# Kernel tuning notes

Hardware: AMD Instinct MI355X
Metric: run time of the kernel (lower is better)

## Reference

```python
import jax, jax.numpy as jnp
import numpy as np

B, N, C, H = 8, 1025, 768, 12
HD = C // H  # 64
SCALE = HD ** -0.5


def rotate_half(x):
    x1, x2 = jnp.split(x, 2, axis=-1)
    return jnp.concatenate((-x2, x1), axis=-1)


def apply_rope(x, sin, cos):
    return x * cos + rotate_half(x) * sin


def setup_inputs() -> dict:
    key = jax.random.key(0)
    ks = jax.random.split(key, 7)
    x = jax.random.normal(ks[0], (B, N, C), dtype=jnp.float32)
    sin = jax.random.normal(ks[1], (N - 1, HD), dtype=jnp.float32)
    cos = jax.random.normal(ks[2], (N - 1, HD), dtype=jnp.float32)
    s = 1.0 / np.sqrt(C)
    qkv_w = jax.random.normal(ks[3], (3 * C, C), dtype=jnp.float32) * s
    qkv_b = jnp.zeros((3 * C,), dtype=jnp.float32)
    proj_w = jax.random.normal(ks[4], (C, C), dtype=jnp.float32) * s
    proj_b = jnp.zeros((C,), dtype=jnp.float32)
    return {"x": x, "sin": sin, "cos": cos, "qkv_w": qkv_w, "qkv_b": qkv_b,
            "proj_w": proj_w, "proj_b": proj_b}


def reference(x, sin, cos, qkv_w, qkv_b, proj_w, proj_b):
    b, n, c = x.shape
    qkv = x @ qkv_w.T + qkv_b                      # [B,N,3C]
    qkv = qkv.reshape(b, n, 3, H, HD)
    qkv = jnp.transpose(qkv, (2, 0, 3, 1, 4))      # [3,B,H,N,HD]
    q, k, v = qkv[0], qkv[1], qkv[2]
    # RoPE on patch tokens only (cls token at index 0 excluded)
    q_patch = apply_rope(q[:, :, 1:, :], sin, cos)
    k_patch = apply_rope(k[:, :, 1:, :], sin, cos)
    q = jnp.concatenate((q[:, :, :1, :], q_patch), axis=2)
    k = jnp.concatenate((k[:, :, :1, :], k_patch), axis=2)
    attn = jnp.einsum('bhqd,bhkd->bhqk', q, k) * SCALE
    attn = jax.nn.softmax(attn, axis=-1)
    out = jnp.einsum('bhqk,bhkd->bhqd', attn, v)   # [B,H,N,HD]
    out = jnp.transpose(out, (0, 2, 1, 3)).reshape(b, n, c)
    out = out @ proj_w.T + proj_b
    return out
```

## Files before the change

### kernel.cpp

```cpp
#include <hip/hip_runtime.h>
#include <hip/hip_bf16.h>

constexpr int NTOK   = 1025;
constexpr int M      = 8 * NTOK;
constexpr int MP     = 8320;
constexpr int KDIM   = 768;
constexpr int NQKV   = 2304;
constexpr int NKVPAD = 1088;
constexpr float SCALEL2 = 0.125f * 1.44269504f;

using bf16x8 = __attribute__((ext_vector_type(8))) short;
using f32x4  = __attribute__((ext_vector_type(4))) float;

__device__ __forceinline__ f32x4 mfma_bf16(bf16x8 a, bf16x8 b, f32x4 c) {
  return __builtin_amdgcn_mfma_f32_16x16x32_bf16(a, b, c, 0, 0, 0);
}

__device__ __forceinline__ void gl16(const void* g, void* l) {
  __builtin_amdgcn_global_load_lds(
      (const __attribute__((address_space(1))) void*)g,
      (__attribute__((address_space(3))) void*)l, 16, 0, 0);
}

template <int N> __device__ __forceinline__ void wait_vmcnt() {
  if constexpr (N == 0)
    asm volatile("s_waitcnt vmcnt(0)" ::: "memory");
  else if constexpr (N == 4)
    asm volatile("s_waitcnt vmcnt(4)" ::: "memory");
  else if constexpr (N == 6)
    asm volatile("s_waitcnt vmcnt(6)" ::: "memory");
}

__device__ __forceinline__ float exp2_raw(float x) {
  float r;
  asm("v_exp_f32 %0, %1" : "=v"(r) : "v"(x));
  return r;
}
__device__ __forceinline__ __hip_bfloat16 cvt_bf16_raw(float x) {
  unsigned u;
  asm("v_cvt_pk_bf16_f32 %0, %1, %2" : "=v"(u) : "v"(x), "v"(x));
  union { unsigned short s; __hip_bfloat16 b; } c;
  c.s = (unsigned short)(u & 0xffffu);
  return c.b;
}

constexpr size_t SZ_X     = (size_t)MP * KDIM * 2;
constexpr size_t SZ_WQ    = (size_t)NQKV * KDIM * 2;
constexpr size_t SZ_PW    = (size_t)KDIM * KDIM * 2;
constexpr size_t SZ_QK    = (size_t)96 * NTOK * 64 * 2;
constexpr size_t SZ_VT    = (size_t)96 * 64 * NKVPAD * 2;
constexpr size_t OFF_XHI  = 0;
constexpr size_t OFF_XLO  = OFF_XHI + SZ_X;
constexpr size_t OFF_WQHI = OFF_XLO + SZ_X;
constexpr size_t OFF_PWHI = OFF_WQHI + SZ_WQ;
constexpr size_t OFF_PWLO = OFF_PWHI + SZ_PW;
constexpr size_t OFF_Q    = OFF_PWLO + SZ_PW;
constexpr size_t OFF_K    = OFF_Q + SZ_QK;
constexpr size_t OFF_VT   = OFF_K + SZ_QK;
constexpr size_t OFF_AO   = OFF_VT + SZ_VT;

__global__ void k_split(const float* __restrict__ src, __hip_bfloat16* __restrict__ hi,
                        __hip_bfloat16* __restrict__ lo, int n_src, int n_dst) {
  int i = blockIdx.x * 256 + threadIdx.x;
  if (i >= n_dst) return;
  float v = (i < n_src) ? src[i] : 0.0f;
  __hip_bfloat16 h = __float2bfloat16(v);
  hi[i] = h;
  lo[i] = __float2bfloat16(v - __bfloat162float(h));
}

__global__ void k_tobf16(const float* __restrict__ src, __hip_bfloat16* __restrict__ dst,
                         int n_src, int n_dst) {
  int i = blockIdx.x * 256 + threadIdx.x;
  if (i >= n_dst) return;
  dst[i] = __float2bfloat16((i < n_src) ? src[i] : 0.0f);
}

__global__ void k_zero_vt(__hip_bfloat16* __restrict__ vt) {
  int i = blockIdx.x * 256 + threadIdx.x;
  constexpr int NPADC = NKVPAD - NTOK;
  if (i >= 96 * 64 * NPADC) return;
  int r = i / NPADC;
  int c = NTOK + (i - r * NPADC);
  vt[(size_t)r * NKVPAD + c] = __float2bfloat16(0.0f);
}

template <int EPI, int NT, int NBX>
__global__ __launch_bounds__(256) void k_gemm(
    const __hip_bfloat16* __restrict__ Ahi, const __hip_bfloat16* __restrict__ Asec,
    const __hip_bfloat16* __restrict__ Bhi, const float* __restrict__ bias,
    const float* __restrict__ sinp, const float* __restrict__ cosp,
    __hip_bfloat16* __restrict__ o_q, __hip_bfloat16* __restrict__ o_k,
    __hip_bfloat16* __restrict__ o_vt, float* __restrict__ o_f32) {
  const int tid = threadIdx.x;
  const int w = tid >> 6, lane = tid & 63;
  const int wm = w >> 1, wn = w & 1;
  const int l15 = lane & 15, q4 = lane >> 4;

  const int nwg = gridDim.x;
  const int orig = blockIdx.x;
  const int qc = nwg >> 3, rc = nwg & 7;
  const int xcd = orig & 7, o8 = orig >> 3;
  const int wg =
      (xcd < rc ? xcd * (qc + 1) : rc * (qc + 1) + (xcd - rc) * qc) + o8;
  const int bx = wg % NBX, by = wg / NBX;
  const int mBase = by * 128, nBase = bx * 128;

  __shared__ __hip_bfloat16 sm[3][NT * 4096];
  constexpr int OFFB = (NT - 1) * 8192;

  const char* p0 = (const char*)Ahi + (size_t)mBase * (KDIM * 2);
  const char* p1 = (const char*)Asec + (size_t)nBase * (KDIM * 2);
  const char* p2 = (const char*)Bhi + (size_t)nBase * (KDIM * 2);

  const int slog = ((tid & 3) ^ ((tid >> 3) & 3)) << 4;
  const int ph = ((q4 ^ ((l15 >> 1) & 3)) << 4);

  auto stage = [&](int kt, int buf) {
    const int kofs = kt * 64;
    char* base = (char*)sm[buf];
#pragma unroll
    for (int i = 0; i < 2; ++i) {
      const int c = i * 256 + tid;
      const size_t rb = (size_t)(i * 64 + (tid >> 2)) * (KDIM * 2) + slog + kofs;
      gl16(p0 + rb, base + (size_t)c * 16);
      if (NT == 3) gl16(p1 + rb, base + 8192 + (size_t)c * 16);
      gl16(p2 + rb, base + OFFB + (size_t)c * 16);
    }
  };

  f32x4 acc[4][4] = {};

  stage(0, 0);
  stage(1, 1);

  constexpr int NKT = KDIM / 32;
  for (int kt = 0; kt < NKT; ++kt) {
    if (kt < NKT - 1)
      wait_vmcnt<2 * NT>();
    else
      wait_vmcnt<0>();
    __builtin_amdgcn_s_barrier();
    if (kt + 2 < NKT) stage(kt + 2, (kt + 2) % 3);
    char* s0 = (char*)sm[kt % 3];
    char* s1 = s0 + 8192;
    char* s2 = s0 + OFFB;
    bf16x8 a0[4], b0[4], b1[4];
#pragma unroll
    for (int mt = 0; mt < 4; ++mt) {
      const int r = wm * 64 + mt * 16 + l15;
      a0[mt] = *(const bf16x8*)(s0 + r * 64 + ph);
    }
#pragma unroll
    for (int nt = 0; nt < 4; ++nt) {
      const int r = wn * 64 + nt * 16 + l15;
      b0[nt] = *(const bf16x8*)(s2 + r * 64 + ph);
      if (NT == 3) b1[nt] = *(const bf16x8*)(s1 + r * 64 + ph);
    }
    __builtin_amdgcn_s_setprio(1);
#pragma unroll
    for (int mt = 0; mt < 4; ++mt)
#pragma unroll
      for (int nt = 0; nt < 4; ++nt) {
        acc[mt][nt] = mfma_bf16(a0[mt], b0[nt], acc[mt][nt]);
        if (NT == 3) acc[mt][nt] = mfma_bf16(a0[mt], b1[nt], acc[mt][nt]);
      }
    __builtin_amdgcn_s_setprio(0);
  }

#pragma unroll
  for (int mt = 0; mt < 4; ++mt)
#pragma unroll
    for (int j = 0; j < 4; ++j) {
      const int gm = mBase + wm * 64 + mt * 16 + q4 * 4 + j;
      if (gm >= M) continue;
      if (EPI == 0) {
        const int b = gm / NTOK;
        const int t = gm - b * NTOK;
#pragma unroll
        for (int nt = 0; nt < 4; ++nt) {
          const int gc = nBase + wn * 64 + nt * 16 + l15;
          float v = acc[mt][nt][j] + bias[gc];
          const int three = gc / 768;
          const int hd = gc - three * 768;
          const int h = hd >> 6, d = hd & 63;
          const int bh = b * 12 + h;
          if (three == 2) {
            o_vt[((size_t)bh * 64 + d) * NKVPAD + t] = __float2bfloat16(v);
          } else {
            if (t > 0) {
              const float pv = acc[mt][nt ^ 2][j] + bias[gc ^ 32];
              const int so = (t - 1) * 64 + d;
              v = v * cosp[so] + ((d < 32) ? -pv : pv) * sinp[so];
            }
            if (three == 0)
              o_q[((size_t)bh * NTOK + t) * 64 + d] = __float2bfloat16(v);
            else
              o_k[((size_t)bh * NTOK + t) * 64 + d] = __float2bfloat16(v * SCALEL2);
          }
        }
      } else {
#pragma unroll
        for (int nt = 0; nt < 4; ++nt) {
          const int gc = nBase + wn * 64 + nt * 16 + l15;
          o_f32[(size_t)gm * 768 + gc] = acc[mt][nt][j] + bias[gc];
        }
      }
    }
}

__global__ __launch_bounds__(256) void k_attn(
    const __hip_bfloat16* __restrict__ Q, const __hip_bfloat16* __restrict__ Kk,
    const __hip_bfloat16* __restrict__ VT, __hip_bfloat16* __restrict__ ao) {
  __shared__ __hip_bfloat16 Kt[3][64 * 64];
  __shared__ __hip_bfloat16 Vt[3][64 * 64];
  __shared__ __hip_bfloat16 Pl[4][32][72];
  const int tid = threadIdx.x, w = tid >> 6, lane = tid & 63;
  const int l15 = lane & 15, q4 = lane >> 4;
  const int id = blockIdx.x;
  const int xcd = id & 7, sub = id >> 3;
  const int hh = sub / 9;
  const int bh = xcd * 12 + hh;
  const int qb = (sub - hh * 9) * 128 + w * 32;
  const size_t qbase = (size_t)bh * NTOK * 64;
  const char* Kb = (const char*)(Kk + qbase);
  const char* Vb = (const char*)(VT + (size_t)bh * 64 * NKVPAD);

  int frag_off[2][4];
#pragma unroll
  for (int f = 0; f < 4; ++f) {
    const int row = f * 16 + l15;
#pragma unroll
    for (int ks = 0; ks < 2; ++ks)
      frag_off[ks][f] = row * 128 + (((ks * 4 + q4) ^ (row & 7)) << 4);
  }
  int stRow[2], sch16[2], stK[2], stV[2], ldsOff[2];
#pragma unroll
  for (int i = 0; i < 2; ++i) {
    const int c = i * 256 + tid;
    const int row = c >> 3;
    stRow[i] = row;
    sch16[i] = ((c & 7) ^ (row & 7)) << 4;
    stK[i] = row * 128 + sch16[i];
    stV[i] = row * (NKVPAD * 2) + sch16[i];
    ldsOff[i] = c * 16;
  }
  int pw_off[2][4], pa_off[2][2];
#pragma unroll
  for (int mt = 0; mt < 2; ++mt) {
#pragma unroll
    for (int j = 0; j < 4; ++j)
      pw_off[mt][j] = ((w * 32 + mt * 16 + q4 * 4 + j) * 72 + l15) * 2;
#pragma unroll
    for (int ks = 0; ks < 2; ++ks)
      pa_off[mt][ks] = ((w * 32 + mt * 16 + l15) * 72 + ks * 32 + q4 * 8) * 2;
  }
  char* Plc = (char*)&Pl[0][0][0];

  bf16x8 qa[2][2];
#pragma unroll
  for (int mt = 0; mt < 2; ++mt) {
    int t = qb + mt * 16 + l15;
    if (t > NTOK - 1) t = NTOK - 1;
#pragma unroll
    for (int ks = 0; ks < 2; ++ks)
      qa[mt][ks] = *(const bf16x8*)(Q + qbase + (size_t)t * 64 + ks * 32 + q4 * 8);
  }

  f32x4 accO[2][4] = {};
  float mrun[2][4], lpart[2][4];
#pragma unroll
  for (int mt = 0; mt < 2; ++mt)
#pragma unroll
    for (int j = 0; j < 4; ++j) {
      mrun[mt][j] = -1e30f;
      lpart[mt][j] = 0.0f;
    }

  auto stageKV = [&](int kt, int b) {
    const int kb0 = kt * 64;
#pragma unroll
    for (int i = 0; i < 2; ++i) {
      const char* srcK;
      if (kt == 16) {
        const int srow = min(kb0 + stRow[i], NTOK - 1);
        srcK = Kb + (size_t)srow * 128 + sch16[i];
      } else {
        srcK = Kb + (size_t)kb0 * 128 + stK[i];
      }
      gl16(srcK, (char*)&Kt[b][0] + ldsOff[i]);
      gl16(Vb + (size_t)kb0 * 2 + stV[i], (char*)&Vt[b][0] + ldsOff[i]);
    }
  };

  auto step = [&](int kt, int cur, bool last) {
    f32x4 s[2][4] = {};
    {
      const char* Kc = (const char*)&Kt[cur][0];
      bf16x8 kfr[2][4];
#pragma unroll
      for (int nt = 0; nt < 4; ++nt)
#pragma unroll
        for (int ks = 0; ks < 2; ++ks)
          kfr[ks][nt] = *(const bf16x8*)(Kc + frag_off[ks][nt]);
      __builtin_amdgcn_s_setprio(1);
#pragma unroll
      for (int mt = 0; mt < 2; ++mt)
#pragma unroll
        for (int nt = 0; nt < 4; ++nt)
#pragma unroll
          for (int ks = 0; ks < 2; ++ks)
            s[mt][nt] = mfma_bf16(qa[mt][ks], kfr[ks][nt], s[mt][nt]);
      __builtin_amdgcn_s_setprio(0);
    }
    if (last) {
#pragma unroll
      for (int nt = 0; nt < 4; ++nt)
        if (1024 + nt * 16 + l15 > NTOK - 1) {
#pragma unroll
          for (int mt = 0; mt < 2; ++mt)
#pragma unroll
            for (int j = 0; j < 4; ++j) s[mt][nt][j] = -1e30f;
        }
    }
    float smax[2][4];
    bool okl = true;
#pragma unroll
    for (int mt = 0; mt < 2; ++mt)
#pragma unroll
      for (int j = 0; j < 4; ++j) {
        const float a =
            fmaxf(fmaxf(s[mt][0][j], s[mt][1][j]), fmaxf(s[mt][2][j], s[mt][3][j]));
        smax[mt][j] = a;
        okl = okl && (a <= mrun[mt][j] + 8.0f);
      }
    if (!__all((int)okl)) {
#pragma unroll
      for (int mt = 0; mt < 2; ++mt)
#pragma unroll
        for (int j = 0; j < 4; ++j) {
          float m0 = smax[mt][j];
#pragma unroll
          for (int off = 1; off < 16; off <<= 1) m0 = fmaxf(m0, __shfl_xor(m0, off));
          const float mnew = fmaxf(mrun[mt][j], m0);
          const float fsc = exp2_raw(mrun[mt][j] - mnew);
          lpart[mt][j] *= fsc;
          mrun[mt][j] = mnew;
#pragma unroll
          for (int nd = 0; nd < 4; ++nd) accO[mt][nd][j] *= fsc;
        }
    }
#pragma unroll
    for (int mt = 0; mt < 2; ++mt)
#pragma unroll
      for (int j = 0; j < 4; ++j) {
        float acc = 0.0f;
        char* pw = Plc + pw_off[mt][j];
#pragma unroll
        for (int nt = 0; nt < 4; ++nt) {
          const float p = exp2_raw(s[mt][nt][j] - mrun[mt][j]);
          acc += p;
          *(__hip_bfloat16*)(pw + nt * 32) = cvt_bf16_raw(p);
        }
        lpart[mt][j] += acc;
      }
    bf16x8 pa[2][2], vf[2][4];
#pragma unroll
    for (int mt = 0; mt < 2; ++mt)
#pragma unroll
      for (int ks = 0; ks < 2; ++ks)
        pa[mt][ks] = *(const bf16x8*)(Plc + pa_off[mt][ks]);
    {
      const char* Vc = (const char*)&Vt[cur][0];
#pragma unroll
      for (int nd = 0; nd < 4; ++nd)
#pragma unroll
        for (int ks = 0; ks < 2; ++ks)
          vf[ks][nd] = *(const bf16x8*)(Vc + frag_off[ks][nd]);
    }
    __builtin_amdgcn_s_setprio(1);
#pragma unroll
    for (int mt = 0; mt < 2; ++mt)
#pragma unroll
      for (int nd = 0; nd < 4; ++nd)
#pragma unroll
        for (int ks = 0; ks < 2; ++ks)
          accO[mt][nd] = mfma_bf16(pa[mt][ks], vf[ks][nd], accO[mt][nd]);
    __builtin_amdgcn_s_setprio(0);
  };

  stageKV(0, 0);
  stageKV(1, 1);
  for (int kt = 0; kt < 17; ++kt) {
    if (kt < 16)
      wait_vmcnt<4>();
    else
      wait_vmcnt<0>();
    __builtin_amdgcn_s_barrier();
    if (kt + 2 < 17) stageKV(kt + 2, (kt + 2) % 3);
    step(kt, kt % 3, kt == 16);
  }

  const int b = bh / 12, h = bh - (bh / 12) * 12;
#pragma unroll
  for (int mt = 0; mt < 2; ++mt)
#pragma unroll
    for (int j = 0; j < 4; ++j) {
      float sum = lpart[mt][j];
#pragma unroll
      for (int off2 = 1; off2 < 16; off2 <<= 1) sum += __shfl_xor(sum, off2);
      const int t = qb + mt * 16 + q4 * 4 + j;
      if (t > NTOK - 1) continue;
      const float inv = 1.0f / sum;
      const size_t ro = ((size_t)(b * NTOK + t)) * 768 + h * 64;
#pragma unroll
      for (int nd = 0; nd < 4; ++nd) {
        const int d = nd * 16 + l15;
        ao[ro + d] = __float2bfloat16(accO[mt][nd][j] * inv);
      }
    }
}

extern "C" void kernel_launch(void* const* d_in, const int* in_sizes, int n_in,
                              void* d_out, int out_size, void* d_ws, size_t ws_size,
                              hipStream_t stream) {
  const float* x = (const float*)d_in[0];
  const float* sinp = (const float*)d_in[1];
  const float* cosp = (const float*)d_in[2];
  const float* qkvw = (const float*)d_in[3];
  const float* qkvb = (const float*)d_in[4];
  const float* projw = (const float*)d_in[5];
  const float* projb = (const float*)d_in[6];

  char* ws = (char*)d_ws;
  __hip_bfloat16* xhi = (__hip_bfloat16*)(ws + OFF_XHI);
  __hip_bfloat16* wqhi = (__hip_bfloat16*)(ws + OFF_WQHI);
  __hip_bfloat16* pwhi = (__hip_bfloat16*)(ws + OFF_PWHI);
  __hip_bfloat16* pwlo = (__hip_bfloat16*)(ws + OFF_PWLO);
  __hip_bfloat16* qb = (__hip_bfloat16*)(ws + OFF_Q);
  __hip_bfloat16* kb = (__hip_bfloat16*)(ws + OFF_K);
  __hip_bfloat16* vt = (__hip_bfloat16*)(ws + OFF_VT);
  __hip_bfloat16* ao = (__hip_bfloat16*)(ws + OFF_AO);

  {
    int n_src = M * KDIM, n_dst = MP * KDIM;
    k_tobf16<<<(n_dst + 255) / 256, 256, 0, stream>>>(x, xhi, n_src, n_dst);
    int nw = NQKV * KDIM;
    k_tobf16<<<(nw + 255) / 256, 256, 0, stream>>>(qkvw, wqhi, nw, nw);
    int np = KDIM * KDIM;
    k_split<<<(np + 255) / 256, 256, 0, stream>>>(projw, pwhi, pwlo, np, np);
    int nz = 96 * 64 * (NKVPAD - NTOK);
    k_zero_vt<<<(nz + 255) / 256, 256, 0, stream>>>(vt);
  }
  k_gemm<0, 2, 18><<<dim3(18 * 65), 256, 0, stream>>>(
      xhi, xhi, wqhi, qkvb, sinp, cosp, qb, kb, vt, nullptr);
  k_attn<<<dim3(864), 256, 0, stream>>>(qb, kb, vt, ao);
  k_gemm<1, 3, 6><<<dim3(6 * 65), 256, 0, stream>>>(
      ao, pwlo, pwhi, projb, nullptr, nullptr, nullptr, nullptr, nullptr,
      (float*)d_out);
}
```

Measured before the change: 223.0 us.

## Fuse prep kernels into one vectorized pass and retile QKV GEMM with K=64 stages

```diff
diff --git a/kernel.cpp b/kernel.cpp
--- a/kernel.cpp
+++ b/kernel.cpp
@@ -36,11 +36,14 @@
   asm("v_exp_f32 %0, %1" : "=v"(r) : "v"(x));
   return r;
 }
-__device__ __forceinline__ __hip_bfloat16 cvt_bf16_raw(float x) {
+__device__ __forceinline__ unsigned short cvt_bf16_u16(float x) {
   unsigned u;
   asm("v_cvt_pk_bf16_f32 %0, %1, %2" : "=v"(u) : "v"(x), "v"(x));
+  return (unsigned short)(u & 0xffffu);
+}
+__device__ __forceinline__ __hip_bfloat16 cvt_bf16_raw(float x) {
   union { unsigned short s; __hip_bfloat16 b; } c;
-  c.s = (unsigned short)(u & 0xffffu);
+  c.s = cvt_bf16_u16(x);
   return c.b;
 }
 
@@ -59,39 +62,67 @@
 constexpr size_t OFF_VT   = OFF_K + SZ_QK;
 constexpr size_t OFF_AO   = OFF_VT + SZ_VT;
 
-__global__ void k_split(const float* __restrict__ src, __hip_bfloat16* __restrict__ hi,
-                        __hip_bfloat16* __restrict__ lo, int n_src, int n_dst) {
-  int i = blockIdx.x * 256 + threadIdx.x;
-  if (i >= n_dst) return;
-  float v = (i < n_src) ? src[i] : 0.0f;
-  __hip_bfloat16 h = __float2bfloat16(v);
-  hi[i] = h;
-  lo[i] = __float2bfloat16(v - __bfloat162float(h));
-}
-
-__global__ void k_tobf16(const float* __restrict__ src, __hip_bfloat16* __restrict__ dst,
-                         int n_src, int n_dst) {
-  int i = blockIdx.x * 256 + threadIdx.x;
-  if (i >= n_dst) return;
-  dst[i] = __float2bfloat16((i < n_src) ? src[i] : 0.0f);
-}
-
-__global__ void k_zero_vt(__hip_bfloat16* __restrict__ vt) {
-  int i = blockIdx.x * 256 + threadIdx.x;
-  constexpr int NPADC = NKVPAD - NTOK;
-  if (i >= 96 * 64 * NPADC) return;
-  int r = i / NPADC;
-  int c = NTOK + (i - r * NPADC);
-  vt[(size_t)r * NKVPAD + c] = __float2bfloat16(0.0f);
-}
-
-template <int EPI, int NT, int NBX>
-__global__ __launch_bounds__(256) void k_gemm(
-    const __hip_bfloat16* __restrict__ Ahi, const __hip_bfloat16* __restrict__ Asec,
-    const __hip_bfloat16* __restrict__ Bhi, const float* __restrict__ bias,
-    const float* __restrict__ sinp, const float* __restrict__ cosp,
-    __hip_bfloat16* __restrict__ o_q, __hip_bfloat16* __restrict__ o_k,
-    __hip_bfloat16* __restrict__ o_vt, float* __restrict__ o_f32) {
+constexpr int N4_X  = MP * KDIM / 4;
+constexpr int N4_WQ = NQKV * KDIM / 4;
+constexpr int N4_PW = KDIM * KDIM / 4;
+constexpr int NPADC = NKVPAD - NTOK;
+constexpr int N4_PAD = 96 * 64 * NPADC / 4;
+constexpr int N4_TOT = N4_X + N4_WQ + N4_PW + N4_PAD;
+
+__global__ void k_prep(const float* __restrict__ x, const float* __restrict__ qkvw,
+                       const float* __restrict__ projw,
+                       __hip_bfloat16* __restrict__ xhi,
+                       __hip_bfloat16* __restrict__ wqhi,
+                       __hip_bfloat16* __restrict__ pwhi,
+                       __hip_bfloat16* __restrict__ pwlo,
+                       __hip_bfloat16* __restrict__ vt) {
+  const int u = blockIdx.x * 256 + threadIdx.x;
+  if (u < N4_X) {
+    const int i = u * 4;
+    ushort4 o = {0, 0, 0, 0};
+    if (i < M * KDIM) {
+      const float4 v = *(const float4*)(x + i);
+      o = ushort4{cvt_bf16_u16(v.x), cvt_bf16_u16(v.y), cvt_bf16_u16(v.z),
+                  cvt_bf16_u16(v.w)};
+    }
+    *(ushort4*)((unsigned short*)xhi + i) = o;
+  } else if (u < N4_X + N4_WQ) {
+    const int i = (u - N4_X) * 4;
+    const float4 v = *(const float4*)(qkvw + i);
+    *(ushort4*)((unsigned short*)wqhi + i) = ushort4{
+        cvt_bf16_u16(v.x), cvt_bf16_u16(v.y), cvt_bf16_u16(v.z), cvt_bf16_u16(v.w)};
+  } else if (u < N4_X + N4_WQ + N4_PW) {
+    const int i = (u - N4_X - N4_WQ) * 4;
+    const float4 v = *(const float4*)(projw + i);
+    float vv[4] = {v.x, v.y, v.z, v.w};
+    unsigned short h[4], l[4];
+#pragma unroll
+    for (int k = 0; k < 4; ++k) {
+      h[k] = cvt_bf16_u16(vv[k]);
+      union { unsigned ui; float f; } c;
+      c.ui = (unsigned)h[k] << 16;
+      l[k] = cvt_bf16_u16(vv[k] - c.f);
+    }
+    *(ushort4*)((unsigned short*)pwhi + i) = ushort4{h[0], h[1], h[2], h[3]};
+    *(ushort4*)((unsigned short*)pwlo + i) = ushort4{l[0], l[1], l[2], l[3]};
+  } else {
+    const int e0 = (u - N4_X - N4_WQ - N4_PW) * 4;
+#pragma unroll
+    for (int k = 0; k < 4; ++k) {
+      const int e = e0 + k;
+      const int r = e / NPADC;
+      const int c = NTOK + (e - r * NPADC);
+      vt[(size_t)r * NKVPAD + c] = __float2bfloat16(0.0f);
+    }
+  }
+}
+
+template <int NBX>
+__global__ __launch_bounds__(256) void k_gemm_qkv(
+    const __hip_bfloat16* __restrict__ A, const __hip_bfloat16* __restrict__ B,
+    const float* __restrict__ bias, const float* __restrict__ sinp,
+    const float* __restrict__ cosp, __hip_bfloat16* __restrict__ o_q,
+    __hip_bfloat16* __restrict__ o_k, __hip_bfloat16* __restrict__ o_vt) {
   const int tid = threadIdx.x;
   const int w = tid >> 6, lane = tid & 63;
   const int wm = w >> 1, wn = w & 1;
@@ -106,8 +137,122 @@
   const int bx = wg % NBX, by = wg / NBX;
   const int mBase = by * 128, nBase = bx * 128;
 
-  __shared__ __hip_bfloat16 sm[3][NT * 4096];
-  constexpr int OFFB = (NT - 1) * 8192;
+  __shared__ __hip_bfloat16 sm[2][2][128 * 64];
+  const char* pA = (const char*)A + (size_t)mBase * 1536;
+  const char* pB = (const char*)B + (size_t)nBase * 1536;
+
+  int stSrc[4], stDst[4];
+#pragma unroll
+  for (int i = 0; i < 4; ++i) {
+    const int c = i * 256 + tid;
+    const int row = c >> 3;
+    stSrc[i] = row * 1536 + (((c & 7) ^ (row & 7)) << 4);
+    stDst[i] = c << 4;
+  }
+  auto stage = [&](int kt, int buf) {
+    const int kofs = kt * 128;
+#pragma unroll
+    for (int i = 0; i < 4; ++i) {
+      gl16(pA + stSrc[i] + kofs, (char*)&sm[buf][0][0] + stDst[i]);
+      gl16(pB + stSrc[i] + kofs, (char*)&sm[buf][1][0] + stDst[i]);
+    }
+  };
+
+  int fA[2][4], fB[2][4];
+#pragma unroll
+  for (int f = 0; f < 4; ++f) {
+    const int ra = wm * 64 + f * 16 + l15;
+    const int rb = wn * 64 + f * 16 + l15;
+#pragma unroll
+    for (int ks = 0; ks < 2; ++ks) {
+      fA[ks][f] = ra * 128 + (((ks * 4 + q4) ^ (ra & 7)) << 4);
+      fB[ks][f] = rb * 128 + (((ks * 4 + q4) ^ (rb & 7)) << 4);
+    }
+  }
+
+  f32x4 acc[4][4] = {};
+
+  stage(0, 0);
+  __syncthreads();
+
+  for (int kt = 0; kt < 12; ++kt) {
+    const int cur = kt & 1;
+    if (kt < 11) stage(kt + 1, cur ^ 1);
+    const char* sA = (const char*)&sm[cur][0][0];
+    const char* sB = (const char*)&sm[cur][1][0];
+    bf16x8 a[2][4], b[2][4];
+#pragma unroll
+    for (int ks = 0; ks < 2; ++ks)
+#pragma unroll
+      for (int f = 0; f < 4; ++f) {
+        a[ks][f] = *(const bf16x8*)(sA + fA[ks][f]);
+        b[ks][f] = *(const bf16x8*)(sB + fB[ks][f]);
+      }
+    __builtin_amdgcn_s_setprio(1);
+#pragma unroll
+    for (int mt = 0; mt < 4; ++mt)
+#pragma unroll
+      for (int nt = 0; nt < 4; ++nt) {
+        acc[mt][nt] = mfma_bf16(a[0][mt], b[0][nt], acc[mt][nt]);
+        acc[mt][nt] = mfma_bf16(a[1][mt], b[1][nt], acc[mt][nt]);
+      }
+    __builtin_amdgcn_s_setprio(0);
+    __syncthreads();
+  }
+
+#pragma unroll
+  for (int mt = 0; mt < 4; ++mt)
+#pragma unroll
+    for (int j = 0; j < 4; ++j) {
+      const int gm = mBase + wm * 64 + mt * 16 + q4 * 4 + j;
+      if (gm >= M) continue;
+      const int b = gm / NTOK;
+      const int t = gm - b * NTOK;
+#pragma unroll
+      for (int nt = 0; nt < 4; ++nt) {
+        const int gc = nBase + wn * 64 + nt * 16 + l15;
+        float v = acc[mt][nt][j] + bias[gc];
+        const int three = gc / 768;
+        const int hd = gc - three * 768;
+        const int h = hd >> 6, d = hd & 63;
+        const int bh = b * 12 + h;
+        if (three == 2) {
+          o_vt[((size_t)bh * 64 + d) * NKVPAD + t] = __float2bfloat16(v);
+        } else {
+          if (t > 0) {
+            const float pv = acc[mt][nt ^ 2][j] + bias[gc ^ 32];
+            const int so = (t - 1) * 64 + d;
+            v = v * cosp[so] + ((d < 32) ? -pv : pv) * sinp[so];
+          }
+          if (three == 0)
+            o_q[((size_t)bh * NTOK + t) * 64 + d] = __float2bfloat16(v);
+          else
+            o_k[((size_t)bh * NTOK + t) * 64 + d] = __float2bfloat16(v * SCALEL2);
+        }
+      }
+    }
+}
+
+template <int NBX>
+__global__ __launch_bounds__(256) void k_gemm_proj(
+    const __hip_bfloat16* __restrict__ Ahi, const __hip_bfloat16* __restrict__ Asec,
+    const __hip_bfloat16* __restrict__ Bhi, const float* __restrict__ bias,
+    float* __restrict__ o_f32) {
+  const int tid = threadIdx.x;
+  const int w = tid >> 6, lane = tid & 63;
+  const int wm = w >> 1, wn = w & 1;
+  const int l15 = lane & 15, q4 = lane >> 4;
+
+  const int nwg = gridDim.x;
+  const int orig = blockIdx.x;
+  const int qc = nwg >> 3, rc = nwg & 7;
+  const int xcd = orig & 7, o8 = orig >> 3;
+  const int wg =
+      (xcd < rc ? xcd * (qc + 1) : rc * (qc + 1) + (xcd - rc) * qc) + o8;
+  const int bx = wg % NBX, by = wg / NBX;
+  const int mBase = by * 128, nBase = bx * 128;
+
+  __shared__ __hip_bfloat16 sm[3][3 * 4096];
 
   const char* p0 = (const char*)Ahi + (size_t)mBase * (KDIM * 2);
   const char* p1 = (const char*)Asec + (size_t)nBase * (KDIM * 2);
@@ -124,8 +269,8 @@
       const int c = i * 256 + tid;
       const size_t rb = (size_t)(i * 64 + (tid >> 2)) * (KDIM * 2) + slog + kofs;
       gl16(p0 + rb, base + (size_t)c * 16);
-      if (NT == 3) gl16(p1 + rb, base + 8192 + (size_t)c * 16);
-      gl16(p2 + rb, base + OFFB + (size_t)c * 16);
+      gl16(p1 + rb, base + 8192 + (size_t)c * 16);
+      gl16(p2 + rb, base + 16384 + (size_t)c * 16);
     }
   };
 
@@ -137,14 +282,14 @@
   constexpr int NKT = KDIM / 32;
   for (int kt = 0; kt < NKT; ++kt) {
     if (kt < NKT - 1)
-      wait_vmcnt<2 * NT>();
+      wait_vmcnt<6>();
     else
       wait_vmcnt<0>();
     __builtin_amdgcn_s_barrier();
     if (kt + 2 < NKT) stage(kt + 2, (kt + 2) % 3);
     char* s0 = (char*)sm[kt % 3];
     char* s1 = s0 + 8192;
-    char* s2 = s0 + OFFB;
+    char* s2 = s0 + 16384;
     bf16x8 a0[4], b0[4], b1[4];
 #pragma unroll
     for (int mt = 0; mt < 4; ++mt) {
@@ -155,7 +300,7 @@
     for (int nt = 0; nt < 4; ++nt) {
       const int r = wn * 64 + nt * 16 + l15;
       b0[nt] = *(const bf16x8*)(s2 + r * 64 + ph);
-      if (NT == 3) b1[nt] = *(const bf16x8*)(s1 + r * 64 + ph);
+      b1[nt] = *(const bf16x8*)(s1 + r * 64 + ph);
     }
     __builtin_amdgcn_s_setprio(1);
 #pragma unroll
@@ -163,7 +308,7 @@
 #pragma unroll
       for (int nt = 0; nt < 4; ++nt) {
         acc[mt][nt] = mfma_bf16(a0[mt], b0[nt], acc[mt][nt]);
-        if (NT == 3) acc[mt][nt] = mfma_bf16(a0[mt], b1[nt], acc[mt][nt]);
+        acc[mt][nt] = mfma_bf16(a0[mt], b1[nt], acc[mt][nt]);
       }
     __builtin_amdgcn_s_setprio(0);
   }
@@ -174,37 +319,10 @@
     for (int j = 0; j < 4; ++j) {
       const int gm = mBase + wm * 64 + mt * 16 + q4 * 4 + j;
       if (gm >= M) continue;
-      if (EPI == 0) {
-        const int b = gm / NTOK;
-        const int t = gm - b * NTOK;
-#pragma unroll
-        for (int nt = 0; nt < 4; ++nt) {
-          const int gc = nBase + wn * 64 + nt * 16 + l15;
-          float v = acc[mt][nt][j] + bias[gc];
-          const int three = gc / 768;
-          const int hd = gc - three * 768;
-          const int h = hd >> 6, d = hd & 63;
-          const int bh = b * 12 + h;
-          if (three == 2) {
-            o_vt[((size_t)bh * 64 + d) * NKVPAD + t] = __float2bfloat16(v);
-          } else {
-            if (t > 0) {
-              const float pv = acc[mt][nt ^ 2][j] + bias[gc ^ 32];
-              const int so = (t - 1) * 64 + d;
-              v = v * cosp[so] + ((d < 32) ? -pv : pv) * sinp[so];
-            }
-            if (three == 0)
-              o_q[((size_t)bh * NTOK + t) * 64 + d] = __float2bfloat16(v);
-            else
-              o_k[((size_t)bh * NTOK + t) * 64 + d] = __float2bfloat16(v * SCALEL2);
-          }
-        }
-      } else {
-#pragma unroll
-        for (int nt = 0; nt < 4; ++nt) {
-          const int gc = nBase + wn * 64 + nt * 16 + l15;
-          o_f32[(size_t)gm * 768 + gc] = acc[mt][nt][j] + bias[gc];
-        }
+#pragma unroll
+      for (int nt = 0; nt < 4; ++nt) {
+        const int gc = nBase + wn * 64 + nt * 16 + l15;
+        o_f32[(size_t)gm * 768 + gc] = acc[mt][nt][j] + bias[gc];
       }
     }
 }
@@ -442,20 +560,11 @@
   __hip_bfloat16* vt = (__hip_bfloat16*)(ws + OFF_VT);
   __hip_bfloat16* ao = (__hip_bfloat16*)(ws + OFF_AO);
 
-  {
-    int n_src = M * KDIM, n_dst = MP * KDIM;
-    k_tobf16<<<(n_dst + 255) / 256, 256, 0, stream>>>(x, xhi, n_src, n_dst);
-    int nw = NQKV * KDIM;
-    k_tobf16<<<(nw + 255) / 256, 256, 0, stream>>>(qkvw, wqhi, nw, nw);
-    int np = KDIM * KDIM;
-    k_split<<<(np + 255) / 256, 256, 0, stream>>>(projw, pwhi, pwlo, np, np);
-    int nz = 96 * 64 * (NKVPAD - NTOK);
-    k_zero_vt<<<(nz + 255) / 256, 256, 0, stream>>>(vt);
-  }
-  k_gemm<0, 2, 18><<<dim3(18 * 65), 256, 0, stream>>>(
-      xhi, xhi, wqhi, qkvb, sinp, cosp, qb, kb, vt, nullptr);
+  k_prep<<<N4_TOT / 256, 256, 0, stream>>>(x, qkvw, projw, xhi, wqhi, pwhi, pwlo,
+                                           vt);
+  k_gemm_qkv<18><<<dim3(18 * 65), 256, 0, stream>>>(xhi, wqhi, qkvb, sinp, cosp,
+                                                    qb, kb, vt);
   k_attn<<<dim3(864), 256, 0, stream>>>(qb, kb, vt, ao);
-  k_gemm<1, 3, 6><<<dim3(6 * 65), 256, 0, stream>>>(
-      ao, pwlo, pwhi, projb, nullptr, nullptr, nullptr, nullptr, nullptr,
-      (float*)d_out);
-}
+  k_gemm_proj<6><<<dim3(6 * 65), 256, 0, stream>>>(ao, pwlo, pwhi, projb,
+                                                   (float*)d_out);
+}
```

After: 223.3 us. Within noise of the previous version (+0.1%).
